# Performance work log

Hardware: AMD Instinct MI355X
Metric: run time of the kernel (lower is better)

The kernel has to match this reference:

```python
import jax, jax.numpy as jnp
import numpy as np

N, E, D, R = 50000, 600000, 128, 8


def rgcn_conv(x, ei, et, W, root, bias):
    # PyG RGCNConv with aggr='mean', root_weight=True, bias=True.
    src, dst = ei[0], ei[1]
    # per-relation transform of all node features: [N, R, D]
    xw = jnp.einsum('nd,rde->nre', x, W)
    msg = xw[src, et]                      # [E, D] gather per edge
    seg = dst * R + et                     # segment per (node, relation)
    summed = jax.ops.segment_sum(msg, seg, num_segments=N * R)
    cnt = jax.ops.segment_sum(jnp.ones((msg.shape[0],), x.dtype), seg,
                              num_segments=N * R)
    mean = summed / jnp.maximum(cnt, 1.0)[:, None]
    agg = mean.reshape(N, R, D).sum(axis=1)  # sum over relations
    return agg + x @ root + bias


def setup_inputs() -> dict:
    key = jax.random.key(0)
    ks = jax.random.split(key, 9)
    s = 1.0 / np.sqrt(D)
    x = jax.random.normal(ks[0], (N, D), jnp.float32)
    ei = jax.random.randint(ks[1], (2, E), 0, N, jnp.int32)
    et = jax.random.randint(ks[2], (E,), 0, R, jnp.int32)
    W1 = jax.random.normal(ks[3], (R, D, D), jnp.float32) * s
    root1 = jax.random.normal(ks[4], (D, D), jnp.float32) * s
    b1 = jnp.zeros((D,), jnp.float32)
    W2 = jax.random.normal(ks[5], (R, D, D), jnp.float32) * s
    root2 = jax.random.normal(ks[6], (D, D), jnp.float32) * s
    b2 = jnp.zeros((D,), jnp.float32)
    rel_emb = jax.random.normal(ks[7], (R, D), jnp.float32)
    return {"x": x, "ei": ei, "et": et, "W1": W1, "root1": root1, "b1": b1,
            "W2": W2, "root2": root2, "b2": b2, "rel_emb": rel_emb}


def reference(x, ei, et, W1, root1, b1, W2, root2, b2, rel_emb):
    h = jax.nn.relu(rgcn_conv(x, ei, et, W1, root1, b1))
    h = jax.nn.relu(rgcn_conv(h, ei, et, W2, root2, b2))
    return (h, rel_emb)
```

## Files before the change

### kernel.cpp

```cpp
#include <hip/hip_runtime.h>
#include <stdint.h>

#define N_NODES 50000
#define N_EDGES 600000
#define N_REL   8
#define NPLANE  9
#define NPAD    50048
#define RCAP    16
#define ZROW    N_NODES
#define PLSZ    (NPAD * 256u)

typedef short v8s __attribute__((ext_vector_type(8)));
typedef float v4f __attribute__((ext_vector_type(4)));
typedef float v2f __attribute__((ext_vector_type(2)));
typedef unsigned short u16;
typedef unsigned int   u32;
typedef __attribute__((address_space(1))) const u32 gas_u32;
typedef __attribute__((address_space(3))) u32 las_u32;

__device__ __forceinline__ float bf2f(u16 u) {
    union { u32 i; float f; } t; t.i = ((u32)u) << 16; return t.f;
}
__device__ __forceinline__ u16 f2bf(float f) {
    union { float f; u32 i; } t; t.f = f;
    u32 lsb = (t.i >> 16) & 1u;
    t.i += 0x7fffu + lsb;
    return (u16)(t.i >> 16);
}
__device__ __forceinline__ v2f bfpair(u32 g) {
    union { u32 i; float f; } a, b;
    a.i = g << 16; b.i = g & 0xffff0000u;
    return (v2f){a.f, b.f};
}
__device__ __forceinline__ float load_f(const void* p, int i, int fl) {
    return fl ? bf2f(((const u16*)p)[i]) : ((const float*)p)[i];
}
__device__ __forceinline__ int wave_detect(const u32* __restrict__ x32) {
    u32 w = x32[threadIdx.x & 63];
    u32 e = (w >> 7) & 0xffu;
    unsigned long long m = __ballot(e >= 112u && e < 144u);
    return __popcll(m) >= 32;
}

#define B_CF    2344
#define B_CONV  (B_CF + 3125)
#define B_PREPW (B_CONV + 1153)
#define B_RELEMB (B_PREPW + 5)
__global__ void k_prep(const void* __restrict__ x, const int* __restrict__ ei,
                       const int* __restrict__ et,
                       const void* __restrict__ W1, const void* __restrict__ r1,
                       const void* __restrict__ b1, const void* __restrict__ W2,
                       const void* __restrict__ r2, const void* __restrict__ b2,
                       const void* __restrict__ rel_emb,
                       u16* __restrict__ xc, u16* __restrict__ hbuf,
                       u16* __restrict__ Wt,
                       u16* __restrict__ bc, int* __restrict__ cnt,
                       u16* __restrict__ evalF, void* __restrict__ out) {
    int b = blockIdx.x, tid = threadIdx.x;
    int fl = wave_detect((const u32*)x);
    if (b < B_CF) {
        int i = b * 256 + tid;
        if (i < N_EDGES) {
            int d = ei[N_EDGES + i];
            int bkt = d * N_REL + et[i];
            int pos = atomicAdd(&cnt[bkt], 1);
            if (pos < RCAP) evalF[(size_t)bkt * RCAP + pos] = (u16)ei[i];
        }
    } else if (b < B_CONV) {
        int g = (b - B_CF) * 256 + tid;
        if (fl) {
            ((int4*)xc)[g] = ((const int4*)x)[g];
        } else {
            const float* xf = (const float*)x + g * 8;
            u16 o[8];
            #pragma unroll
            for (int j = 0; j < 8; ++j) o[j] = f2bf(xf[j]);
            *(int4*)(xc + g * 8) = *(const int4*)o;
        }
    } else if (b < B_PREPW) {
        int o = (b - B_CONV) * 256 + tid;
        if (o < 2 * NPLANE * 16384) {
            int l = o / (NPLANE * 16384);
            int rem = o - l * (NPLANE * 16384);
            int rr = rem >> 14;
            int j = (rem >> 7) & 127;
            int k = rem & 127;
            float v = (rr < 8)
                ? load_f(l ? W2 : W1, rr * 16384 + k * 128 + j, fl)
                : load_f(l ? r2 : r1, k * 128 + j, fl);
            Wt[o] = f2bf(v);
        } else if (o < 2 * NPLANE * 16384 + 256) {
            int o2 = o - 2 * NPLANE * 16384;
            bc[o2] = f2bf(load_f((o2 >> 7) ? b2 : b1, o2 & 127, fl));
        }
    } else if (b < B_PREPW + 4) {
        int i = (b - B_PREPW) * 256 + tid;
        if (i < N_REL * 128) {
            size_t o = (size_t)N_NODES * 128 + i;
            if (fl) ((u16*)out)[o]   = ((const u16*)rel_emb)[i];
            else    ((float*)out)[o] = ((const float*)rel_emb)[i];
        }
    } else {
        if (tid < 64)        ((u32*)(xc   + (size_t)ZROW * 128))[tid]      = 0;
        else if (tid < 128)  ((u32*)(hbuf + (size_t)ZROW * 128))[tid - 64] = 0;
    }
}

__global__ __launch_bounds__(512, 4) void k_gemmT(
        const u16* __restrict__ feat,
        const u16* __restrict__ Wt,
        u16* __restrict__ Y) {
    __shared__ __align__(16) u16 As[128 * 128];
    __shared__ __align__(16) u16 Bs[128 * 128];
    int tid = threadIdx.x;
    int bx = blockIdx.x;
    int mb = bx / 9, rp = bx - mb * 9;
    int bm0 = mb * 128;
    int wave = tid >> 6, lane = tid & 63;
    int wm = (wave & 3) * 32, wn = (wave >> 2) * 64;
    int lrow = lane & 15, quad = lane >> 4;

    v4f accr[2][4];
    #pragma unroll
    for (int i = 0; i < 2; ++i)
        #pragma unroll
        for (int j = 0; j < 4; ++j) accr[i][j] = (v4f){0.f, 0.f, 0.f, 0.f};

    #pragma unroll
    for (int j = 0; j < 4; ++j) {
        int off = wave * 4096 + j * 1024 + lane * 16;
        int row = off >> 8;
        int cc = ((off >> 4) & 15) ^ (row & 15);
        __builtin_amdgcn_global_load_lds(
            (gas_u32*)(feat + (size_t)(bm0 + row) * 128 + cc * 8),
            (las_u32*)(As + (off >> 1) - lane * 8), 16, 0, 0);
        __builtin_amdgcn_global_load_lds(
            (gas_u32*)(Wt + ((rp * 128 + row) << 7) + cc * 8),
            (las_u32*)(Bs + (off >> 1) - lane * 8), 16, 0, 0);
    }
    __syncthreads();

    #pragma unroll
    for (int kk = 0; kk < 4; ++kk) {
        int chunk = kk * 4 + quad;
        v8s a[2], b[4];
        #pragma unroll
        for (int t = 0; t < 2; ++t) {
            int row = wm + t * 16 + lrow;
            a[t] = *(const v8s*)(As + row * 128 + (chunk ^ (row & 15)) * 8);
        }
        #pragma unroll
        for (int t = 0; t < 4; ++t) {
            int row = wn + t * 16 + lrow;
            b[t] = *(const v8s*)(Bs + row * 128 + (chunk ^ (row & 15)) * 8);
        }
        #pragma unroll
        for (int ti = 0; ti < 2; ++ti)
            #pragma unroll
            for (int tj = 0; tj < 4; ++tj)
                accr[ti][tj] = __builtin_amdgcn_mfma_f32_16x16x32_bf16(a[ti], b[tj], accr[ti][tj], 0, 0, 0);
    }

    u16* yp = Y + ((size_t)rp * NPAD + bm0) * 128;
    #pragma unroll
    for (int ti = 0; ti < 2; ++ti)
        #pragma unroll
        for (int reg = 0; reg < 4; ++reg) {
            int rloc = wm + ti * 16 + quad * 4 + reg;
            #pragma unroll
            for (int tj = 0; tj < 4; ++tj) {
                int col = wn + tj * 16 + lrow;
                yp[(size_t)rloc * 128 + col] = f2bf(accr[ti][tj][reg]);
            }
        }
}

__global__ __launch_bounds__(256) void k_out(
        const u16* __restrict__ Y,
        const int* __restrict__ cnt, const u16* __restrict__ evalF,
        const u16* __restrict__ bias,
        const u32* __restrict__ xdet,
        u16* __restrict__ hout, void* __restrict__ fout, int final_out) {
    int wave = threadIdx.x >> 6, lane = threadIdx.x & 63;
    int node = blockIdx.x * 4 + wave;
    if (node >= N_NODES) return;
    int fl = wave_detect(xdet);
    u32 lane4 = (u32)lane * 4u;
    int base = node * N_REL;

    int4 ca = ((const int4*)(cnt + base))[0];
    int4 cb = ((const int4*)(cnt + base))[1];
    int cs[8] = {ca.x, ca.y, ca.z, ca.w, cb.x, cb.y, cb.z, cb.w};
    const u16* eb = evalF + (size_t)base * RCAP;
    ushort4 eg[8];
    #pragma unroll
    for (int r = 0; r < N_REL; ++r)
        eg[r] = *(const ushort4*)(eb + r * RCAP);

    const char* fb = (const char*)Y;
    v2f acc[N_REL];
    #pragma unroll
    for (int r = 0; r < N_REL; ++r) {
        int c = cs[r];
        u32 pb = (u32)r * PLSZ;
        u32 o0 = pb + ((u32)(c > 0 ? (int)eg[r].x : ZROW) << 8) + lane4;
        u32 o1 = pb + ((u32)(c > 1 ? (int)eg[r].y : ZROW) << 8) + lane4;
        u32 o2 = pb + ((u32)(c > 2 ? (int)eg[r].z : ZROW) << 8) + lane4;
        u32 o3 = pb + ((u32)(c > 3 ? (int)eg[r].w : ZROW) << 8) + lane4;
        u32 g0 = *(const u32*)(fb + o0);
        u32 g1 = *(const u32*)(fb + o1);
        u32 g2 = *(const u32*)(fb + o2);
        u32 g3 = *(const u32*)(fb + o3);
        acc[r] = (bfpair(g0) + bfpair(g1)) + (bfpair(g2) + bfpair(g3));
    }

    int cmax = cs[0];
    #pragma unroll
    for (int r = 1; r < N_REL; ++r) cmax = cs[r] > cmax ? cs[r] : cmax;
    if (cmax > 4) {
        #pragma unroll
        for (int r = 0; r < N_REL; ++r) {
            int c = cs[r] < RCAP ? cs[r] : RCAP;
            for (int j = 4; j < c; ++j) {
                u32 oj = (u32)r * PLSZ + ((u32)eb[r * RCAP + j] << 8) + lane4;
                acc[r] += bfpair(*(const u32*)(fb + oj));
            }
        }
    }

    v2f sum = bfpair(*(const u32*)(fb + 8u * PLSZ + ((u32)node << 8) + lane4));
    sum += bfpair(*(const u32*)((const char*)bias + lane4));
    #pragma unroll
    for (int r = 0; r < N_REL; ++r) {
        int cc = cs[r] < RCAP ? cs[r] : RCAP;
        if (cc < 1) cc = 1;
        float inv = __builtin_amdgcn_rcpf((float)cc);
        sum.x += acc[r].x * inv;
        sum.y += acc[r].y * inv;
    }
    float sx = fmaxf(sum.x, 0.f), sy = fmaxf(sum.y, 0.f);
    size_t oidx = (size_t)node * 128 + lane * 2;
    if (!final_out) {
        u32 pk;
        asm("v_cvt_pk_bf16_f32 %0, %1, %2" : "=v"(pk) : "v"(sx), "v"(sy));
        *(u32*)(hout + oidx) = pk;
    } else if (fl) {
        u32 pk;
        asm("v_cvt_pk_bf16_f32 %0, %1, %2" : "=v"(pk) : "v"(sx), "v"(sy));
        *(u32*)((u16*)fout + oidx) = pk;
    } else {
        ((float*)fout)[oidx]     = sx;
        ((float*)fout)[oidx + 1] = sy;
    }
}

static inline size_t align_up(size_t x, size_t a) { return (x + a - 1) & ~(a - 1); }

extern "C" void kernel_launch(void* const* d_in, const int* in_sizes, int n_in,
                              void* d_out, int out_size, void* d_ws, size_t ws_size,
                              hipStream_t stream) {
    const int* ei = (const int*)d_in[1];
    const int* et = (const int*)d_in[2];

    char* ws = (char*)d_ws;
    size_t off = 0;
    u16* Wt     = (u16*)(ws + off);  off = align_up(off + (size_t)2 * NPLANE * 16384 * 2, 256);
    u16* bc     = (u16*)(ws + off);  off = align_up(off + 512, 256);
    u16* xc     = (u16*)(ws + off);  off = align_up(off + (size_t)NPAD * 128 * 2, 256);
    int* cnt    = (int*)(ws + off);  off = align_up(off + (size_t)N_NODES * N_REL * 4, 256);
    u16* evalF  = (u16*)(ws + off);  off = align_up(off + (size_t)N_NODES * N_REL * RCAP * 2, 256);
    u16* h      = (u16*)(ws + off);  off = align_up(off + (size_t)NPAD * 128 * 2, 256);
    u16* Y      = (u16*)(ws + off);  off += (size_t)NPLANE * NPAD * 128 * 2;
    (void)in_sizes; (void)n_in; (void)out_size; (void)ws_size;

    hipMemsetAsync(cnt, 0, (size_t)N_NODES * N_REL * 4, stream);
    k_prep<<<B_RELEMB, 256, 0, stream>>>(d_in[0], ei, et, d_in[3], d_in[4], d_in[5],
                                         d_in[6], d_in[7], d_in[8], d_in[9],
                                         xc, h, Wt, bc, cnt, evalF, d_out);

    for (int l = 0; l < 2; ++l) {
        const u16* src = l ? h : xc;
        k_gemmT<<<(NPAD / 128) * 9, 512, 0, stream>>>(src, Wt + (size_t)l * NPLANE * 16384, Y);
        k_out<<<(N_NODES + 3) / 4, 256, 0, stream>>>(Y, cnt, evalF, bc + l * 128,
                                                     (const u32*)d_in[0], h, d_out, l);
    }
}
```

Measured before the change: 263.5 us.

## Fuse edge bucketing into first GEMM launch and zero counts in prep kernel

```diff
diff --git a/kernel.cpp b/kernel.cpp
--- a/kernel.cpp
+++ b/kernel.cpp
@@ -9,6 +9,8 @@
 #define RCAP    16
 #define ZROW    N_NODES
 #define PLSZ    (NPAD * 256u)
+#define NGEMMB  ((NPAD / 128) * 9)
+#define NCFB    1172
 
 typedef short v8s __attribute__((ext_vector_type(8)));
 typedef float v4f __attribute__((ext_vector_type(4)));
@@ -42,32 +44,25 @@
     return __popcll(m) >= 32;
 }
 
-#define B_CF    2344
-#define B_CONV  (B_CF + 3125)
+#define B_ZC    391
+#define B_CONV  (B_ZC + 3125)
 #define B_PREPW (B_CONV + 1153)
-#define B_RELEMB (B_PREPW + 5)
-__global__ void k_prep(const void* __restrict__ x, const int* __restrict__ ei,
-                       const int* __restrict__ et,
-                       const void* __restrict__ W1, const void* __restrict__ r1,
-                       const void* __restrict__ b1, const void* __restrict__ W2,
-                       const void* __restrict__ r2, const void* __restrict__ b2,
-                       const void* __restrict__ rel_emb,
-                       u16* __restrict__ xc, u16* __restrict__ hbuf,
-                       u16* __restrict__ Wt,
-                       u16* __restrict__ bc, int* __restrict__ cnt,
-                       u16* __restrict__ evalF, void* __restrict__ out) {
+#define B_TOTAL (B_PREPW + 5)
+__global__ void k_prepA(const void* __restrict__ x,
+                        const void* __restrict__ W1, const void* __restrict__ r1,
+                        const void* __restrict__ b1, const void* __restrict__ W2,
+                        const void* __restrict__ r2, const void* __restrict__ b2,
+                        const void* __restrict__ rel_emb,
+                        u16* __restrict__ xc, u16* __restrict__ hbuf,
+                        u16* __restrict__ Wt, u16* __restrict__ bc,
+                        int* __restrict__ cnt, void* __restrict__ out) {
     int b = blockIdx.x, tid = threadIdx.x;
     int fl = wave_detect((const u32*)x);
-    if (b < B_CF) {
-        int i = b * 256 + tid;
-        if (i < N_EDGES) {
-            int d = ei[N_EDGES + i];
-            int bkt = d * N_REL + et[i];
-            int pos = atomicAdd(&cnt[bkt], 1);
-            if (pos < RCAP) evalF[(size_t)bkt * RCAP + pos] = (u16)ei[i];
-        }
+    if (b < B_ZC) {
+        int i4 = b * 256 + tid;
+        if (i4 < 100000) ((int4*)cnt)[i4] = (int4){0, 0, 0, 0};
     } else if (b < B_CONV) {
-        int g = (b - B_CF) * 256 + tid;
+        int g = (b - B_ZC) * 256 + tid;
         if (fl) {
             ((int4*)xc)[g] = ((const int4*)x)[g];
         } else {
@@ -106,15 +101,13 @@
     }
 }
 
-__global__ __launch_bounds__(512, 4) void k_gemmT(
-        const u16* __restrict__ feat,
-        const u16* __restrict__ Wt,
+__device__ __forceinline__ void gemmT_body(int gbx,
+        const u16* __restrict__ feat, const u16* __restrict__ Wt,
         u16* __restrict__ Y) {
     __shared__ __align__(16) u16 As[128 * 128];
     __shared__ __align__(16) u16 Bs[128 * 128];
     int tid = threadIdx.x;
-    int bx = blockIdx.x;
-    int mb = bx / 9, rp = bx - mb * 9;
+    int mb = gbx / 9, rp = gbx - mb * 9;
     int bm0 = mb * 128;
     int wave = tid >> 6, lane = tid & 63;
     int wm = (wave & 3) * 32, wn = (wave >> 2) * 64;
@@ -173,6 +166,33 @@
                 yp[(size_t)rloc * 128 + col] = f2bf(accr[ti][tj][reg]);
             }
         }
+}
+
+__global__ __launch_bounds__(512, 4) void k_gemmT_cf(
+        const u16* __restrict__ feat, const u16* __restrict__ Wt,
+        u16* __restrict__ Y,
+        const int* __restrict__ ei, const int* __restrict__ et,
+        int* __restrict__ cnt, u16* __restrict__ evalF) {
+    int bx = blockIdx.x;
+    int phase = bx & 3, quarter = bx >> 2;
+    if (phase == 0 && quarter < NCFB) {
+        int i = quarter * 512 + threadIdx.x;
+        if (i < N_EDGES) {
+            int d = ei[N_EDGES + i];
+            int bkt = d * N_REL + et[i];
+            int pos = atomicAdd(&cnt[bkt], 1);
+            if (pos < RCAP) evalF[(size_t)bkt * RCAP + pos] = (u16)ei[i];
+        }
+        return;
+    }
+    int cfbefore = (quarter >= NCFB) ? NCFB : (quarter + (phase > 0 ? 1 : 0));
+    gemmT_body(bx - cfbefore, feat, Wt, Y);
+}
+
+__global__ __launch_bounds__(512, 4) void k_gemmT(
+        const u16* __restrict__ feat, const u16* __restrict__ Wt,
+        u16* __restrict__ Y) {
+    gemmT_body(blockIdx.x, feat, Wt, Y);
 }
 
 __global__ __launch_bounds__(256) void k_out(
@@ -273,15 +293,13 @@
     u16* Y      = (u16*)(ws + off);  off += (size_t)NPLANE * NPAD * 128 * 2;
     (void)in_sizes; (void)n_in; (void)out_size; (void)ws_size;
 
-    hipMemsetAsync(cnt, 0, (size_t)N_NODES * N_REL * 4, stream);
-    k_prep<<<B_RELEMB, 256, 0, stream>>>(d_in[0], ei, et, d_in[3], d_in[4], d_in[5],
+    k_prepA<<<B_TOTAL, 256, 0, stream>>>(d_in[0], d_in[3], d_in[4], d_in[5],
                                          d_in[6], d_in[7], d_in[8], d_in[9],
-                                         xc, h, Wt, bc, cnt, evalF, d_out);
-
-    for (int l = 0; l < 2; ++l) {
-        const u16* src = l ? h : xc;
-        k_gemmT<<<(NPAD / 128) * 9, 512, 0, stream>>>(src, Wt + (size_t)l * NPLANE * 16384, Y);
-        k_out<<<(N_NODES + 3) / 4, 256, 0, stream>>>(Y, cnt, evalF, bc + l * 128,
-                                                     (const u32*)d_in[0], h, d_out, l);
-    }
-}
+                                         xc, h, Wt, bc, cnt, d_out);
+    k_gemmT_cf<<<NGEMMB + NCFB, 512, 0, stream>>>(xc, Wt, Y, ei, et, cnt, evalF);
+    k_out<<<(N_NODES + 3) / 4, 256, 0, stream>>>(Y, cnt, evalF, bc,
+                                                 (const u32*)d_in[0], h, d_out, 0);
+    k_gemmT<<<NGEMMB, 512, 0, stream>>>(h, Wt + (size_t)NPLANE * 16384, Y);
+    k_out<<<(N_NODES + 3) / 4, 256, 0, stream>>>(Y, cnt, evalF, bc + 128,
+                                                 (const u32*)d_in[0], h, d_out, 1);
+}
```

Result: faster. 256.4 us (-2.7%).
